# Performance work log

Measured on AMD Instinct MI355X. Metric: run time of the kernel, lower is better.

Reference implementation:

```python
import jax, jax.numpy as jnp
import numpy as np

N_NODES = 50000
N_EDGES = 500000
IN_F, HID, EMB = 128, 256, 128

def setup_inputs() -> dict:
    key = jax.random.key(0)
    ks = jax.random.split(key, 9)
    x = jax.random.normal(ks[0], (N_NODES, IN_F), dtype=jnp.float32)
    src = jax.random.randint(ks[1], (N_EDGES,), 0, N_NODES, dtype=jnp.int32)
    dst = jax.random.randint(ks[2], (N_EDGES,), 0, N_NODES, dtype=jnp.int32)
    def lin(k, fan_in, fan_out):
        bound = 1.0 / np.sqrt(fan_in)
        kw, kb = jax.random.split(k)
        W = jax.random.uniform(kw, (fan_in, fan_out), minval=-bound, maxval=bound, dtype=jnp.float32)
        b = jax.random.uniform(kb, (fan_out,), minval=-bound, maxval=bound, dtype=jnp.float32)
        return W, b
    W1, b1 = lin(ks[3], IN_F, HID)
    W2, b2 = lin(ks[4], HID, HID)
    W3, b3 = lin(ks[5], HID, EMB)
    return {"x": x, "src": src, "dst": dst, "W1": W1, "b1": b1,
            "W2": W2, "b2": b2, "W3": W3, "b3": b3}

def _gcn_layer(h, src, dst, W, b):
    # sum messages from src nodes into dst nodes, then linear
    agg = jax.ops.segment_sum(h[src], dst, num_segments=N_NODES)  # [N, F]
    return agg @ W + b

def reference(x, src, dst, W1, b1, W2, b2, W3, b3):
    h = jax.nn.relu(_gcn_layer(x, src, dst, W1, b1))
    h = jax.nn.relu(_gcn_layer(h, src, dst, W2, b2))
    h = _gcn_layer(h, src, dst, W3, b3)
    # dgl.mean_nodes on a single graph: mean of relu(h) over all nodes -> [EMB]
    return jnp.mean(jax.nn.relu(h), axis=0)
```

## Files before the change

### kernel.cpp

```cpp
#include <hip/hip_runtime.h>

#define N_NODES 50000
#define N_EDGES 500000

typedef __attribute__((ext_vector_type(8))) short short8;
typedef __attribute__((ext_vector_type(8))) unsigned short ushort8v;
typedef __attribute__((ext_vector_type(4))) float floatx4;
typedef __attribute__((ext_vector_type(4))) unsigned int uint4v;

__device__ inline float bf2f(unsigned short u) {
    unsigned int x = ((unsigned int)u) << 16;
    return __builtin_bit_cast(float, x);
}
__device__ inline unsigned short f2bf(float f) {
    unsigned int x = __builtin_bit_cast(unsigned int, f);
    x += 0x7fff + ((x >> 16) & 1);
    return (unsigned short)(x >> 16);
}

__device__ __forceinline__ void gld_lds16(const unsigned short* g, unsigned short* l) {
    __builtin_amdgcn_global_load_lds((const __attribute__((address_space(1))) void*)g,
                                     (__attribute__((address_space(3))) void*)l, 16, 0, 0);
}

__device__ inline void accum16B(float2* a, ushort8v rv) {
    uint4v u = __builtin_bit_cast(uint4v, rv);
    #pragma unroll
    for (int p = 0; p < 4; p++) {
        float lo = __builtin_bit_cast(float, u[p] << 16);
        float hi = __builtin_bit_cast(float, u[p] & 0xFFFF0000u);
        a[p].x += lo;
        a[p].y += hi;
    }
}


__global__ __launch_bounds__(256) void histprep_kernel(const int* __restrict__ dst,
                                                       int* __restrict__ deg,
                                                       const float* __restrict__ W1,
                                                       const float* __restrict__ W2,
                                                       const float* __restrict__ W3,
                                                       const float* __restrict__ x,
                                                       unsigned short* __restrict__ Wt1,
                                                       unsigned short* __restrict__ Wt2,
                                                       unsigned short* __restrict__ Wt3,
                                                       unsigned short* __restrict__ xb,
                                                       int* __restrict__ bsum,
                                                       float* __restrict__ outZ) {
    int idx = blockIdx.x * 256 + threadIdx.x;
    if (idx < N_EDGES) { atomicAdd(&deg[dst[idx]], 1); return; }
    idx -= N_EDGES;
    if (idx < 32768) {
        if (idx < 256) bsum[idx] = 0;
        if (idx < 128) outZ[idx] = 0.f;
        int k = idx >> 8, n = idx & 255;
        Wt1[n * 128 + k] = f2bf(W1[idx]);
    } else if (idx < 98304) {
        int i = idx - 32768;
        int k = i >> 8, n = i & 255;
        Wt2[n * 256 + k] = f2bf(W2[i]);
    } else if (idx < 131072) {
        int i = idx - 98304;
        int k = i >> 7, n = i & 127;
        Wt3[n * 256 + k] = f2bf(W3[i]);
    } else {
        int i = (idx - 131072) * 4;
        if (i < N_NODES * 128) {
            float4 v = *(const float4*)(x + i);
            ushort4 o;
            o.x = f2bf(v.x); o.y = f2bf(v.y); o.z = f2bf(v.z); o.w = f2bf(v.w);
            *(ushort4*)(xb + i) = o;
        }
    }
}


__global__ __launch_bounds__(256) void scan_onepass_kernel(int* __restrict__ cur,
                                                           int* __restrict__ bsum,
                                                           int* __restrict__ off, int n) {
    __shared__ int s[256];
    int b = blockIdx.x, t = threadIdx.x;
    int i = b * 256 + t;
    int v = (i < n) ? cur[i] : 0;
    s[t] = v;
    __syncthreads();
    #pragma unroll
    for (int d = 1; d < 256; d <<= 1) {
        int u = (t >= d) ? s[t - d] : 0;
        __syncthreads();
        s[t] += u;
        __syncthreads();
    }
    int incl = s[t];
    if (t == 255) atomicExch(&bsum[b], s[255] + 1);
    int pre = 0;
    if (t < b) {
        volatile int* p = (volatile int*)&bsum[t];
        int vv;
        while ((vv = *p) == 0) { }
        pre = vv - 1;
    }
    __syncthreads();
    s[t] = pre;
    __syncthreads();
    #pragma unroll
    for (int d = 128; d > 0; d >>= 1) {
        if (t < d) s[t] += s[t + d];
        __syncthreads();
    }
    int base = s[0];
    if (i == 0) off[0] = 0;
    if (i < n) {
        int inclG = base + incl;
        off[i + 1] = inclG;
        cur[i] = inclG - v;
    }
}

__global__ void fill_kernel(const int* __restrict__ src, const int* __restrict__ dst,
                            int* __restrict__ cur, int* __restrict__ csr, int nE) {
    int e = blockIdx.x * 256 + threadIdx.x;
    if (e < nE) {
        int p = atomicAdd(&cur[dst[e]], 1);
        csr[p] = src[e];
    }
}


template<int F>
__global__ __launch_bounds__(512) void fused_agg_gemm_kernel(const unsigned short* __restrict__ H,
                                                             const int* __restrict__ off,
                                                             const int* __restrict__ csr,
                                                             const unsigned short* __restrict__ Bt,
                                                             const float* __restrict__ bias,
                                                             unsigned short* __restrict__ C,
                                                             int M) {
    constexpr int BM = 64, BN = 256, BK = 32, KS = F / BK;
    constexpr int LDAF = F + 8;
    constexpr int LPR = F / 8;
    constexpr int G = 512 / LPR;
    __shared__ unsigned short Afull[BM * LDAF];
    __shared__ unsigned short Bs[BN * BK];
    int tid = threadIdx.x;
    int m0 = blockIdx.x * BM;

    #pragma unroll
    for (int it = 0; it < 2; it++) {
        int d = tid + it * 512;
        int r = d >> 2, slot = d & 3;
        int j = (slot - (r >> 1)) & 3;
        gld_lds16(Bt + (size_t)r * F + j * 8, &Bs[d * 8]);
    }

    {
        int gid = tid / LPR, li = tid % LPR;
        int f0 = li * 8;
        for (int n = gid; n < BM; n += G) {
            int node = m0 + n;
            if (node < M) {
                int s = off[node], e = off[node + 1];
                float2 a[4], b[4];
                #pragma unroll
                for (int p = 0; p < 4; p++) {
                    a[p] = make_float2(0.f, 0.f);
                    b[p] = make_float2(0.f, 0.f);
                }
                int i = s;
                for (; i + 8 <= e; i += 8) {
                    ushort8v r[8];
                    #pragma unroll
                    for (int j = 0; j < 8; j++)
                        r[j] = *(const ushort8v*)(H + (size_t)csr[i + j] * F + f0);
                    #pragma unroll
                    for (int j = 0; j < 4; j++) accum16B(a, r[j]);
                    #pragma unroll
                    for (int j = 4; j < 8; j++) accum16B(b, r[j]);
                }
                if (i + 4 <= e) {
                    ushort8v r[4];
                    #pragma unroll
                    for (int j = 0; j < 4; j++)
                        r[j] = *(const ushort8v*)(H + (size_t)csr[i + j] * F + f0);
                    #pragma unroll
                    for (int j = 0; j < 4; j++) accum16B(a, r[j]);
                    i += 4;
                }
                if (i < e) {
                    ushort8v r[4];
                    #pragma unroll
                    for (int j = 0; j < 4; j++) {
                        int ii = i + j < e ? i + j : e - 1;
                        r[j] = *(const ushort8v*)(H + (size_t)csr[ii] * F + f0);
                    }
                    #pragma unroll
                    for (int j = 0; j < 4; j++)
                        if (i + j < e) accum16B(b, r[j]);
                }
                ushort8v o;
                #pragma unroll
                for (int p = 0; p < 4; p++) {
                    o[2 * p]     = f2bf(a[p].x + b[p].x);
                    o[2 * p + 1] = f2bf(a[p].y + b[p].y);
                }
                *(ushort8v*)&Afull[n * LDAF + f0] = o;
            }
        }
    }
    __syncthreads();

    int wave = tid >> 6, lane = tid & 63;
    int wm = wave & 1, wn = wave >> 1;
    int mlane = lane & 15, kgrp = lane >> 4;
    floatx4 acc[2][4];
    #pragma unroll
    for (int i = 0; i < 2; i++)
        #pragma unroll
        for (int j = 0; j < 4; j++) acc[i][j] = (floatx4){0.f, 0.f, 0.f, 0.f};

    for (int ks = 0; ks < KS; ks++) {
        short8 af[2], bfr[4];
        #pragma unroll
        for (int nt = 0; nt < 4; nt++) {
            int r = wn * 64 + nt * 16 + mlane;
            int slot = (kgrp + (r >> 1)) & 3;
            bfr[nt] = *(const short8*)&Bs[r * BK + slot * 8];
        }
        #pragma unroll
        for (int mt = 0; mt < 2; mt++)
            af[mt] = *(const short8*)&Afull[(wm * 32 + mt * 16 + mlane) * LDAF + ks * BK + kgrp * 8];
        __syncthreads();
        if (ks + 1 < KS) {
            #pragma unroll
            for (int it = 0; it < 2; it++) {
                int d = tid + it * 512;
                int r = d >> 2, slot = d & 3;
                int j = (slot - (r >> 1)) & 3;
                gld_lds16(Bt + (size_t)r * F + (ks + 1) * BK + j * 8, &Bs[d * 8]);
            }
        }
        #pragma unroll
        for (int mt = 0; mt < 2; mt++)
            #pragma unroll
            for (int nt = 0; nt < 4; nt++)
                acc[mt][nt] = __builtin_amdgcn_mfma_f32_16x16x32_bf16(af[mt], bfr[nt],
                                                                      acc[mt][nt], 0, 0, 0);
        if (ks + 1 < KS) __syncthreads();
    }
    #pragma unroll
    for (int mt = 0; mt < 2; mt++) {
        #pragma unroll
        for (int nt = 0; nt < 4; nt++) {
            int col = wn * 64 + nt * 16 + mlane;
            float bv = bias[col];
            #pragma unroll
            for (int r = 0; r < 4; r++) {
                int row = m0 + wm * 32 + mt * 16 + kgrp * 4 + r;
                if (row < M) {
                    float v = fmaxf(acc[mt][nt][r] + bv, 0.f);
                    C[(size_t)row * BN + col] = f2bf(v);
                }
            }
        }
    }
}


__device__ inline void agg128_body(const unsigned short* __restrict__ h,
                                   const int* __restrict__ off,
                                   const int* __restrict__ csr,
                                   int node, int quad, int f0, float2* a) {
    int s = __builtin_amdgcn_readfirstlane(off[node]);
    int e = __builtin_amdgcn_readfirstlane(off[node + 1]);
    int i = s;
    for (; i + 8 <= e; i += 8) {
        ushort8v r[2];
        #pragma unroll
        for (int j = 0; j < 2; j++) {
            int base = i + 4 * j;
            int i0 = csr[base], i1 = csr[base + 1], i2 = csr[base + 2], i3 = csr[base + 3];
            int id = quad == 0 ? i0 : quad == 1 ? i1 : quad == 2 ? i2 : i3;
            r[j] = *(const ushort8v*)(h + (size_t)id * 128 + f0);
        }
        #pragma unroll
        for (int j = 0; j < 2; j++) accum16B(a, r[j]);
    }
    int rem = e - i;
    if (rem > 0) {
        int nr = (rem + 3) >> 2;
        ushort8v r[2];
        #pragma unroll
        for (int j = 0; j < 2; j++) {
            if (j < nr) {
                int base = i + 4 * j;
                int c1 = base + 1 < e ? base + 1 : e - 1;
                int c2 = base + 2 < e ? base + 2 : e - 1;
                int c3 = base + 3 < e ? base + 3 : e - 1;
                int i0 = csr[base], i1 = csr[c1], i2 = csr[c2], i3 = csr[c3];
                int id = quad == 0 ? i0 : quad == 1 ? i1 : quad == 2 ? i2 : i3;
                r[j] = *(const ushort8v*)(h + (size_t)id * 128 + f0);
            }
        }
        #pragma unroll
        for (int j = 0; j < 2; j++) {
            if (j < nr && (i + 4 * j + quad) < e) accum16B(a, r[j]);
        }
    }
    #pragma unroll
    for (int p = 0; p < 4; p++) {
        a[p].x += __shfl_xor(a[p].x, 16, 64);
        a[p].y += __shfl_xor(a[p].y, 16, 64);
        a[p].x += __shfl_xor(a[p].x, 32, 64);
        a[p].y += __shfl_xor(a[p].y, 32, 64);
    }
}


__global__ __launch_bounds__(256) void agg3_mean_kernel(const unsigned short* __restrict__ t,
                                                        const int* __restrict__ off,
                                                        const int* __restrict__ csr,
                                                        const float* __restrict__ b3,
                                                        float* __restrict__ partial) {
    __shared__ float sm[4 * 128];
    int wave = threadIdx.x >> 6, lane = threadIdx.x & 63;
    int node = blockIdx.x * 4 + wave;
    int quad = lane >> 4;
    int f0 = (lane & 15) * 8;
    float2 a[4];
    #pragma unroll
    for (int p = 0; p < 4; p++) a[p] = make_float2(0.f, 0.f);
    agg128_body(t, off, csr, node, quad, f0, a);
    if (quad == 0) {
        #pragma unroll
        for (int p = 0; p < 4; p++) {
            sm[wave * 128 + f0 + 2 * p]     = fmaxf(a[p].x + b3[f0 + 2 * p], 0.f);
            sm[wave * 128 + f0 + 2 * p + 1] = fmaxf(a[p].y + b3[f0 + 2 * p + 1], 0.f);
        }
    }
    __syncthreads();
    if (threadIdx.x < 128) {
        int f = threadIdx.x;
        float p = sm[f] + sm[128 + f] + sm[256 + f] + sm[384 + f];
        partial[(size_t)blockIdx.x * 128 + f] = p;
    }
}

__global__ __launch_bounds__(256) void mean_reduce_kernel(const float* __restrict__ partial,
                                                          float* __restrict__ outp, int nRows) {
    __shared__ float s[256];
    int f = threadIdx.x & 127, half = threadIdx.x >> 7;
    int chunk = (nRows + gridDim.x - 1) / gridDim.x;
    int r0 = blockIdx.x * chunk;
    int r1 = r0 + chunk < nRows ? r0 + chunk : nRows;
    float acc = 0.f;
    for (int r = r0 + half; r < r1; r += 2) acc += partial[(size_t)r * 128 + f];
    s[threadIdx.x] = acc;
    __syncthreads();
    if (half == 0) atomicAdd(&outp[f], (s[f] + s[f + 128]) * (1.0f / N_NODES));
}


template<typename T> __device__ inline void storeC(T* p, float v);
template<> __device__ inline void storeC<float>(float* p, float v) { *p = v; }
template<> __device__ inline void storeC<unsigned short>(unsigned short* p, float v) { *p = f2bf(v); }

template<typename OUT_T>
__global__ __launch_bounds__(256) void gemm_bf16_kernel(const unsigned short* __restrict__ A,
                                                        const unsigned short* __restrict__ Bt,
                                                        const float* __restrict__ bias,
                                                        OUT_T* __restrict__ C,
                                                        int M, int K, int N, int doRelu) {
    constexpr int BM = 64, BN = 128, BK = 32;
    __shared__ unsigned short As[BM * BK];
    __shared__ unsigned short Bs[BN * BK];
    int tid = threadIdx.x;
    int m0 = blockIdx.y * BM, n0 = blockIdx.x * BN;
    int wave = tid >> 6, lane = tid & 63;
    int wm = wave >> 1, wn = wave & 1;
    int mlane = lane & 15, kgrp = lane >> 4;

    floatx4 acc[2][4];
    #pragma unroll
    for (int i = 0; i < 2; i++)
        #pragma unroll
        for (int j = 0; j < 4; j++) acc[i][j] = (floatx4){0.f, 0.f, 0.f, 0.f};

    for (int k0 = 0; k0 < K; k0 += BK) {
        {
            int c = tid;
            int r = c >> 2, cb = (c & 3) * 8;
            gld_lds16(A + (size_t)(m0 + r) * K + k0 + cb, &As[c * 8]);
        }
        #pragma unroll
        for (int it = 0; it < 2; it++) {
            int c = tid + it * 256;
            int r = c >> 2, cb = (c & 3) * 8;
            gld_lds16(Bt + (size_t)(n0 + r) * K + k0 + cb, &Bs[c * 8]);
        }
        __syncthreads();
        short8 af[2], bfr[4];
        #pragma unroll
        for (int mt = 0; mt < 2; mt++)
            af[mt] = *(const short8*)&As[(wm * 32 + mt * 16 + mlane) * BK + kgrp * 8];
        #pragma unroll
        for (int nt = 0; nt < 4; nt++)
            bfr[nt] = *(const short8*)&Bs[(wn * 64 + nt * 16 + mlane) * BK + kgrp * 8];
        #pragma unroll
        for (int mt = 0; mt < 2; mt++)
            #pragma unroll
            for (int nt = 0; nt < 4; nt++)
                acc[mt][nt] = __builtin_amdgcn_mfma_f32_16x16x32_bf16(af[mt], bfr[nt],
                                                                      acc[mt][nt], 0, 0, 0);
        __syncthreads();
    }
    #pragma unroll
    for (int mt = 0; mt < 2; mt++) {
        #pragma unroll
        for (int nt = 0; nt < 4; nt++) {
            int col = n0 + wn * 64 + nt * 16 + mlane;
            float bv = bias ? bias[col] : 0.f;
            #pragma unroll
            for (int r = 0; r < 4; r++) {
                int row = m0 + wm * 32 + mt * 16 + kgrp * 4 + r;
                if (row < M) {
                    float v = acc[mt][nt][r] + bv;
                    if (doRelu) v = fmaxf(v, 0.f);
                    storeC(C + (size_t)row * N + col, v);
                }
            }
        }
    }
}


extern "C" void kernel_launch(void* const* d_in, const int* in_sizes, int n_in,
                              void* d_out, int out_size, void* d_ws, size_t ws_size,
                              hipStream_t stream) {
    const float* x   = (const float*)d_in[0];
    const int*   src = (const int*)d_in[1];
    const int*   dst = (const int*)d_in[2];
    const float* W1 = (const float*)d_in[3];
    const float* b1 = (const float*)d_in[4];
    const float* W2 = (const float*)d_in[5];
    const float* b2 = (const float*)d_in[6];
    const float* W3 = (const float*)d_in[7];
    const float* b3 = (const float*)d_in[8];
    float* out = (float*)d_out;

    char* ws = (char*)d_ws;
    size_t o = 0;
    auto alloc = [&](size_t bytes) -> char* {
        char* p = ws + o;
        o = (o + bytes + 255) & ~(size_t)255;
        return p;
    };
    int* off     = (int*)alloc((size_t)(N_NODES + 1) * 4);
    int* cur     = (int*)alloc((size_t)N_NODES * 4);
    int* csrIdx  = (int*)alloc((size_t)N_EDGES * 4);
    int* bsum    = (int*)alloc(256 * 4);
    unsigned short* Wt1 = (unsigned short*)alloc((size_t)128 * 256 * 2);
    unsigned short* Wt2 = (unsigned short*)alloc((size_t)256 * 256 * 2);
    unsigned short* Wt3 = (unsigned short*)alloc((size_t)256 * 128 * 2);
    char* R1 = alloc((size_t)N_NODES * 256 * 2);
    char* R2 = alloc((size_t)N_NODES * 256 * 2);
    char* R3 = alloc((size_t)N_NODES * 256 * 2);
    (void)alloc(65536);

    unsigned short* xb    = (unsigned short*)R1;
    unsigned short* h1    = (unsigned short*)R3;
    unsigned short* h2    = (unsigned short*)R2;
    unsigned short* t     = (unsigned short*)R3;
    float*          pmean = (float*)R1;

    const int nb = (N_NODES + 255) / 256;

    hipMemsetAsync(cur, 0, (size_t)N_NODES * 4, stream);
    const int hpThreads = N_EDGES + 131072 + N_NODES * 128 / 4;
    histprep_kernel<<<(hpThreads + 255) / 256, 256, 0, stream>>>(dst, cur, W1, W2, W3, x,
                                                                 Wt1, Wt2, Wt3, xb, bsum, out);
    scan_onepass_kernel<<<nb, 256, 0, stream>>>(cur, bsum, off, N_NODES);
    fill_kernel<<<(N_EDGES + 255) / 256, 256, 0, stream>>>(src, dst, cur, csrIdx, N_EDGES);

    const int mbF = (N_NODES + 63) / 64;

    fused_agg_gemm_kernel<128><<<mbF, 512, 0, stream>>>(xb, off, csrIdx, Wt1, b1, h1, N_NODES);
    fused_agg_gemm_kernel<256><<<mbF, 512, 0, stream>>>(h1, off, csrIdx, Wt2, b2, h2, N_NODES);
    gemm_bf16_kernel<unsigned short><<<dim3(1, mbF), 256, 0, stream>>>(h2, Wt3, nullptr, t,
                                                                       N_NODES, 256, 128, 0);
    agg3_mean_kernel<<<N_NODES / 4, 256, 0, stream>>>(t, off, csrIdx, b3, pmean);
    mean_reduce_kernel<<<128, 256, 0, stream>>>(pmean, out, N_NODES / 4);
}
```

Measured before the change: 288.4 us.

## Fuse third-layer linear transform into second aggregate-GEMM kernel epilogue

The layer-2 fused aggregation+GEMM kernel now writes its relu output tile into shared memory and immediately multiplies it by W3 using MFMA, emitting t directly. This removes the separate layer-3 GEMM launch and the round trip of the 50000x256 bf16 h2 tensor through global memory. The cost is extra epilogue work and synchronisation per block, with W3 fragments read straight from global/L2 memory rather than staged in LDS.

```diff
diff --git a/kernel.cpp b/kernel.cpp
--- a/kernel.cpp
+++ b/kernel.cpp
@@ -127,13 +127,15 @@
 }
 
 
-template<int F>
+template<int F, bool FUSE_T>
 __global__ __launch_bounds__(512) void fused_agg_gemm_kernel(const unsigned short* __restrict__ H,
                                                              const int* __restrict__ off,
                                                              const int* __restrict__ csr,
                                                              const unsigned short* __restrict__ Bt,
                                                              const float* __restrict__ bias,
                                                              unsigned short* __restrict__ C,
+                                                             const unsigned short* __restrict__ W3t,
+                                                             unsigned short* __restrict__ tOut,
                                                              int M) {
     constexpr int BM = 64, BN = 256, BK = 32, KS = F / BK;
     constexpr int LDAF = F + 8;
@@ -246,18 +248,74 @@
                                                                       acc[mt][nt], 0, 0, 0);
         if (ks + 1 < KS) __syncthreads();
     }
-    #pragma unroll
-    for (int mt = 0; mt < 2; mt++) {
-        #pragma unroll
-        for (int nt = 0; nt < 4; nt++) {
-            int col = wn * 64 + nt * 16 + mlane;
-            float bv = bias[col];
-            #pragma unroll
-            for (int r = 0; r < 4; r++) {
-                int row = m0 + wm * 32 + mt * 16 + kgrp * 4 + r;
-                if (row < M) {
+
+    if (!FUSE_T) {
+        #pragma unroll
+        for (int mt = 0; mt < 2; mt++) {
+            #pragma unroll
+            for (int nt = 0; nt < 4; nt++) {
+                int col = wn * 64 + nt * 16 + mlane;
+                float bv = bias[col];
+                #pragma unroll
+                for (int r = 0; r < 4; r++) {
+                    int row = m0 + wm * 32 + mt * 16 + kgrp * 4 + r;
+                    if (row < M) {
+                        float v = fmaxf(acc[mt][nt][r] + bv, 0.f);
+                        C[(size_t)row * BN + col] = f2bf(v);
+                    }
+                }
+            }
+        }
+    } else {
+        __syncthreads();
+        #pragma unroll
+        for (int mt = 0; mt < 2; mt++) {
+            #pragma unroll
+            for (int nt = 0; nt < 4; nt++) {
+                int col = wn * 64 + nt * 16 + mlane;
+                float bv = bias[col];
+                #pragma unroll
+                for (int r = 0; r < 4; r++) {
+                    int rl = wm * 32 + mt * 16 + kgrp * 4 + r;
                     float v = fmaxf(acc[mt][nt][r] + bv, 0.f);
-                    C[(size_t)row * BN + col] = f2bf(v);
+                    Afull[rl * LDAF + col] = f2bf(v);
+                }
+            }
+        }
+        __syncthreads();
+        int wm2 = wave & 1, wn2 = wave >> 1;
+        floatx4 tacc[2][2];
+        #pragma unroll
+        for (int i = 0; i < 2; i++)
+            #pragma unroll
+            for (int j = 0; j < 2; j++) tacc[i][j] = (floatx4){0.f, 0.f, 0.f, 0.f};
+        for (int ks = 0; ks < 8; ks++) {
+            short8 af2[2], bf2r[2];
+            #pragma unroll
+            for (int nt = 0; nt < 2; nt++)
+                bf2r[nt] = *(const short8*)(W3t + (size_t)(wn2 * 32 + nt * 16 + mlane) * 256
+                                            + ks * 32 + kgrp * 8);
+            #pragma unroll
+            for (int mt = 0; mt < 2; mt++)
+                af2[mt] = *(const short8*)&Afull[(wm2 * 32 + mt * 16 + mlane) * LDAF
+                                                 + ks * 32 + kgrp * 8];
+            #pragma unroll
+            for (int mt = 0; mt < 2; mt++)
+                #pragma unroll
+                for (int nt = 0; nt < 2; nt++)
+                    tacc[mt][nt] = __builtin_amdgcn_mfma_f32_16x16x32_bf16(af2[mt], bf2r[nt],
+                                                                           tacc[mt][nt], 0, 0, 0);
+        }
+        #pragma unroll
+        for (int mt = 0; mt < 2; mt++) {
+            #pragma unroll
+            for (int nt = 0; nt < 2; nt++) {
+                int col = wn2 * 32 + nt * 16 + mlane;
+                #pragma unroll
+                for (int r = 0; r < 4; r++) {
+                    int row = m0 + wm2 * 32 + mt * 16 + kgrp * 4 + r;
+                    if (row < M)
+                        tOut[(size_t)row * 128 + col] = f2bf(tacc[mt][nt][r]);
                 }
             }
         }
@@ -356,79 +414,6 @@
     s[threadIdx.x] = acc;
     __syncthreads();
     if (half == 0) atomicAdd(&outp[f], (s[f] + s[f + 128]) * (1.0f / N_NODES));
-}
-
-
-template<typename T> __device__ inline void storeC(T* p, float v);
-template<> __device__ inline void storeC<float>(float* p, float v) { *p = v; }
-template<> __device__ inline void storeC<unsigned short>(unsigned short* p, float v) { *p = f2bf(v); }
-
-template<typename OUT_T>
-__global__ __launch_bounds__(256) void gemm_bf16_kernel(const unsigned short* __restrict__ A,
-                                                        const unsigned short* __restrict__ Bt,
-                                                        const float* __restrict__ bias,
-                                                        OUT_T* __restrict__ C,
-                                                        int M, int K, int N, int doRelu) {
-    constexpr int BM = 64, BN = 128, BK = 32;
-    __shared__ unsigned short As[BM * BK];
-    __shared__ unsigned short Bs[BN * BK];
-    int tid = threadIdx.x;
-    int m0 = blockIdx.y * BM, n0 = blockIdx.x * BN;
-    int wave = tid >> 6, lane = tid & 63;
-    int wm = wave >> 1, wn = wave & 1;
-    int mlane = lane & 15, kgrp = lane >> 4;
-
-    floatx4 acc[2][4];
-    #pragma unroll
-    for (int i = 0; i < 2; i++)
-        #pragma unroll
-        for (int j = 0; j < 4; j++) acc[i][j] = (floatx4){0.f, 0.f, 0.f, 0.f};
-
-    for (int k0 = 0; k0 < K; k0 += BK) {
-        {
-            int c = tid;
-            int r = c >> 2, cb = (c & 3) * 8;
-            gld_lds16(A + (size_t)(m0 + r) * K + k0 + cb, &As[c * 8]);
-        }
-        #pragma unroll
-        for (int it = 0; it < 2; it++) {
-            int c = tid + it * 256;
-            int r = c >> 2, cb = (c & 3) * 8;
-            gld_lds16(Bt + (size_t)(n0 + r) * K + k0 + cb, &Bs[c * 8]);
-        }
-        __syncthreads();
-        short8 af[2], bfr[4];
-        #pragma unroll
-        for (int mt = 0; mt < 2; mt++)
-            af[mt] = *(const short8*)&As[(wm * 32 + mt * 16 + mlane) * BK + kgrp * 8];
-        #pragma unroll
-        for (int nt = 0; nt < 4; nt++)
-            bfr[nt] = *(const short8*)&Bs[(wn * 64 + nt * 16 + mlane) * BK + kgrp * 8];
-        #pragma unroll
-        for (int mt = 0; mt < 2; mt++)
-            #pragma unroll
-            for (int nt = 0; nt < 4; nt++)
-                acc[mt][nt] = __builtin_amdgcn_mfma_f32_16x16x32_bf16(af[mt], bfr[nt],
-                                                                      acc[mt][nt], 0, 0, 0);
-        __syncthreads();
-    }
-    #pragma unroll
-    for (int mt = 0; mt < 2; mt++) {
-        #pragma unroll
-        for (int nt = 0; nt < 4; nt++) {
-            int col = n0 + wn * 64 + nt * 16 + mlane;
-            float bv = bias ? bias[col] : 0.f;
-            #pragma unroll
-            for (int r = 0; r < 4; r++) {
-                int row = m0 + wm * 32 + mt * 16 + kgrp * 4 + r;
-                if (row < M) {
-                    float v = acc[mt][nt][r] + bv;
-                    if (doRelu) v = fmaxf(v, 0.f);
-                    storeC(C + (size_t)row * N + col, v);
-                }
-            }
-        }
-    }
 }
 
 
@@ -467,8 +452,7 @@
 
     unsigned short* xb    = (unsigned short*)R1;
     unsigned short* h1    = (unsigned short*)R3;
-    unsigned short* h2    = (unsigned short*)R2;
-    unsigned short* t     = (unsigned short*)R3;
+    unsigned short* t     = (unsigned short*)R2;
     float*          pmean = (float*)R1;
 
     const int nb = (N_NODES + 255) / 256;
@@ -482,10 +466,10 @@
 
     const int mbF = (N_NODES + 63) / 64;
 
-    fused_agg_gemm_kernel<128><<<mbF, 512, 0, stream>>>(xb, off, csrIdx, Wt1, b1, h1, N_NODES);
-    fused_agg_gemm_kernel<256><<<mbF, 512, 0, stream>>>(h1, off, csrIdx, Wt2, b2, h2, N_NODES);
-    gemm_bf16_kernel<unsigned short><<<dim3(1, mbF), 256, 0, stream>>>(h2, Wt3, nullptr, t,
-                                                                       N_NODES, 256, 128, 0);
+    fused_agg_gemm_kernel<128, false><<<mbF, 512, 0, stream>>>(xb, off, csrIdx, Wt1, b1, h1,
+                                                               nullptr, nullptr, N_NODES);
+    fused_agg_gemm_kernel<256, true><<<mbF, 512, 0, stream>>>(h1, off, csrIdx, Wt2, b2, nullptr,
+                                                              Wt3, t, N_NODES);
     agg3_mean_kernel<<<N_NODES / 4, 256, 0, stream>>>(t, off, csrIdx, b3, pmean);
     mean_reduce_kernel<<<128, 256, 0, stream>>>(pmean, out, N_NODES / 4);
 }
```

Result: faster. 278.9 us (-3.3%).
